# Kernel tuning notes

Hardware: AMD Instinct MI355X
Metric: run time of the kernel (lower is better)

The kernel has to match this reference:

```python
import jax, jax.numpy as jnp
import numpy as np

LN_EPS = 1e-5
B, T, H = 32, 1024, 1024


def _layer_norm(v, g, b):
    m = v.mean(-1, keepdims=True)
    var = ((v - m) ** 2).mean(-1, keepdims=True)
    return (v - m) / jnp.sqrt(var + LN_EPS) * g + b


def setup_inputs() -> dict:
    key = jax.random.key(0)
    ks = jax.random.split(key, 10)
    s_t = 1.0 / np.sqrt(T)
    s_h = 1.0 / np.sqrt(H)
    return {
        "x": jax.random.normal(ks[0], (B, T, H), jnp.float32),
        # temporal MLP (square T x T, triangular-masked), torch Linear layout [out, in]
        "tw1": jax.random.uniform(ks[1], (T, T), jnp.float32, -s_t, s_t),
        "tb1": jax.random.uniform(ks[2], (T,), jnp.float32, -s_t, s_t),
        "tw2": jax.random.uniform(ks[3], (T, T), jnp.float32, -s_t, s_t),
        "tb2": jax.random.uniform(ks[4], (T,), jnp.float32, -s_t, s_t),
        # channel MLP (square H x H)
        "cw1": jax.random.uniform(ks[5], (H, H), jnp.float32, -s_h, s_h),
        "cb1": jax.random.uniform(ks[6], (H,), jnp.float32, -s_h, s_h),
        "cw2": jax.random.uniform(ks[7], (H, H), jnp.float32, -s_h, s_h),
        "cb2": jax.random.uniform(ks[8], (H,), jnp.float32, -s_h, s_h),
        # LayerNorm affine params
        "ln1_g": jnp.ones((H,), jnp.float32),
        "ln1_b": jnp.zeros((H,), jnp.float32),
        "ln2_g": jnp.ones((H,), jnp.float32),
        "ln2_b": jnp.zeros((H,), jnp.float32),
    }


def reference(x, tw1, tb1, tw2, tb2, cw1, cb1, cw2, cb2, ln1_g, ln1_b, ln2_g, ln2_b):
    t = tw1.shape[0]
    mask = jnp.tril(jnp.ones((t, t), x.dtype))  # diagonal=0: include self
    # temporal mixing: LN -> swap -> masked Linear -> GELU -> masked Linear -> swap
    y = _layer_norm(x, ln1_g, ln1_b)
    y = jnp.swapaxes(y, 1, 2)  # [B, H, T]
    y = y @ (mask * tw1).T + tb1
    y = jax.nn.gelu(y, approximate=False)
    y = y @ (mask * tw2).T + tb2
    y = jnp.swapaxes(y, 1, 2)  # [B, T, H]
    x = x + y
    # channel mixing: LN -> Linear -> GELU -> Linear
    y2 = _layer_norm(x, ln2_g, ln2_b)
    y2 = jax.nn.gelu(y2 @ cw1.T + cb1, approximate=False) @ cw2.T + cb2
    return x + y2
```

## Files before the change

### kernel.cpp

```cpp
#include <hip/hip_runtime.h>
#include <hip/hip_bf16.h>

#define BDIM 32
#define TDIM 1024
#define HDIM 1024

typedef __attribute__((ext_vector_type(8))) short short8;
typedef __attribute__((ext_vector_type(8))) unsigned short ushort8;
typedef __attribute__((ext_vector_type(4))) unsigned short u16x4;
typedef __attribute__((ext_vector_type(4))) float f32x4;

__device__ __forceinline__ float b2f(unsigned short h){ return __uint_as_float(((unsigned)h)<<16); }
__device__ __forceinline__ unsigned short f2b(float f){
  unsigned u = __float_as_uint(f);
  u += 0x7fffu + ((u>>16)&1u);
  return (unsigned short)(u>>16);
}
__device__ __forceinline__ float gelu_f(float v){ return 0.5f*v*(1.0f+erff(v*0.70710678118f)); }
__device__ __forceinline__ void stv(float* p, float v){ *p = v; }
__device__ __forceinline__ void stv(unsigned short* p, float v){ *p = f2b(v); }

__global__ void prep_weights(const float* __restrict__ w1, const float* __restrict__ w2,
                             const float* __restrict__ c1, const float* __restrict__ c2,
                             unsigned short* __restrict__ w1m, unsigned short* __restrict__ w2m,
                             unsigned short* __restrict__ c1b, unsigned short* __restrict__ c2b){
  int idx = blockIdx.x*blockDim.x + threadIdx.x;
  int e = idx*4;
  int i = e >> 10, j0 = e & 1023;
  f32x4 a = *(const f32x4*)(w1+e);
  f32x4 b = *(const f32x4*)(w2+e);
  f32x4 c = *(const f32x4*)(c1+e);
  f32x4 d = *(const f32x4*)(c2+e);
  u16x4 av, bv, cv, dv;
  #pragma unroll
  for (int q=0;q<4;++q){
    float am = (j0+q <= i) ? a[q] : 0.f;
    float bm = (j0+q <= i) ? b[q] : 0.f;
    av[q]=f2b(am); bv[q]=f2b(bm); cv[q]=f2b(c[q]); dv[q]=f2b(d[q]);
  }
  *(u16x4*)(w1m+e)=av; *(u16x4*)(w2m+e)=bv; *(u16x4*)(c1b+e)=cv; *(u16x4*)(c2b+e)=dv;
}

__global__ __launch_bounds__(256) void ln1_stats_transpose(
    const float* __restrict__ x, const float* __restrict__ g, const float* __restrict__ bta,
    unsigned short* __restrict__ xnT){
  __shared__ float sm[64], sr[64];
  __shared__ float tile[64][65];
  const int t0 = blockIdx.x*64;
  const int b  = blockIdx.y;
  const int tid = threadIdx.x, wid = tid>>6, lane = tid&63;
  const size_t base = (size_t)b*TDIM*HDIM;
  for (int rr=0; rr<16; ++rr){
    int r = rr*4 + wid;
    const float* pr = x + base + (size_t)(t0+r)*HDIM;
    float s=0.f, s2=0.f;
    #pragma unroll
    for (int it=0; it<4; ++it){
      f32x4 v = *(const f32x4*)(pr + it*256 + lane*4);
      #pragma unroll
      for (int c=0;c<4;++c){ s += v[c]; s2 += v[c]*v[c]; }
    }
    #pragma unroll
    for (int off=32; off>0; off>>=1){ s += __shfl_xor(s,off,64); s2 += __shfl_xor(s2,off,64); }
    if (lane==0){
      float m = s * (1.0f/HDIM);
      sm[r] = m; sr[r] = rsqrtf(s2*(1.0f/HDIM) - m*m + 1e-5f);
    }
  }
  __syncthreads();
  const int rr = tid>>3, c8 = tid&7;
  for (int ht=0; ht<16; ++ht){
    int h0 = ht*64;
    #pragma unroll
    for (int p=0;p<2;++p){
      int r = rr + p*32;
      float m = sm[r], rs = sr[r];
      f32x4 v0 = *(const f32x4*)(x + base + (size_t)(t0+r)*HDIM + h0 + c8*8);
      f32x4 v1 = *(const f32x4*)(x + base + (size_t)(t0+r)*HDIM + h0 + c8*8 + 4);
      #pragma unroll
      for (int c=0;c<4;++c){
        int h = c8*8+c;
        tile[r][h]   = (v0[c]-m)*rs*g[h0+h]   + bta[h0+h];
        tile[r][h+4] = (v1[c]-m)*rs*g[h0+h+4] + bta[h0+h+4];
      }
    }
    __syncthreads();
    #pragma unroll
    for (int p=0;p<2;++p){
      int hr = rr + p*32;
      ushort8 ov;
      #pragma unroll
      for (int c=0;c<8;++c) ov[c] = f2b(tile[c8*8+c][hr]);
      *(ushort8*)(xnT + base + (size_t)(h0+hr)*TDIM + t0 + c8*8) = ov;
    }
    __syncthreads();
  }
}

__global__ void ln_fused(const unsigned short* __restrict__ p, const float* __restrict__ g,
                         const float* __restrict__ bta, unsigned short* __restrict__ o){
  int wid = threadIdx.x>>6, lane = threadIdx.x&63;
  size_t row = (size_t)blockIdx.x*4 + wid;
  const unsigned short* pr = p + row*HDIM + lane*16;
  ushort8 v0 = *(const ushort8*)(pr);
  ushort8 v1 = *(const ushort8*)(pr+8);
  float f[16];
  float s=0.f, s2=0.f;
  #pragma unroll
  for (int c=0;c<8;++c){ f[c]=b2f(v0[c]); f[c+8]=b2f(v1[c]); }
  #pragma unroll
  for (int c=0;c<16;++c){ s += f[c]; s2 += f[c]*f[c]; }
  #pragma unroll
  for (int off=32; off>0; off>>=1){ s += __shfl_xor(s,off,64); s2 += __shfl_xor(s2,off,64); }
  float m = s * (1.0f/HDIM);
  float rs = rsqrtf(s2*(1.0f/HDIM) - m*m + 1e-5f);
  int h0 = lane*16;
  ushort8 o0, o1;
  #pragma unroll
  for (int c=0;c<8;++c){
    o0[c] = f2b((f[c]-m)*rs*g[h0+c] + bta[h0+c]);
    o1[c] = f2b((f[c+8]-m)*rs*g[h0+c+8] + bta[h0+c+8]);
  }
  *(ushort8*)(o + row*HDIM + h0) = o0;
  *(ushort8*)(o + row*HDIM + h0 + 8) = o1;
}

template<int MODE, typename CT, typename RT>
__global__ __launch_bounds__(512,2)
void gemm256(const unsigned short* __restrict__ act, const unsigned short* __restrict__ wgt,
             CT* __restrict__ C, const float* __restrict__ bias, const RT* __restrict__ resid){
  extern __shared__ short S[];
  const int bid = blockIdx.x;
  const int tile = (bid & 7)*64 + (bid >> 3);
  const int panel = tile >> 2;
  const int inner = tile & 3;
  const unsigned short *pa, *pb;
  size_t cbase; int rg0, cg0, kend;
  if constexpr (MODE==1){
    int b = panel>>2, mt = panel&3;
    pa = act + (size_t)b*1048576 + (size_t)mt*262144;
    pb = wgt + (size_t)inner*262144;
    kend = (inner+1)*256;
    cbase = (size_t)b*1048576; rg0 = mt*256; cg0 = inner*256;
  } else if constexpr (MODE==2){
    int b = panel>>2, nt = panel&3;
    pa = wgt + (size_t)inner*262144;
    pb = act + (size_t)b*1048576 + (size_t)nt*262144;
    kend = (inner+1)*256;
    cbase = (size_t)b*1048576; rg0 = inner*256; cg0 = nt*256;
  } else {
    pa = act + (size_t)panel*262144;
    pb = wgt + (size_t)inner*262144;
    kend = 1024;
    cbase = 0; rg0 = panel*256; cg0 = inner*256;
  }
  const int tid = threadIdx.x;
  const int lane = tid & 63, wid = tid >> 6;
  const int wr = wid >> 2, wc = wid & 3;
  f32x4 acc[8][4];
  #pragma unroll
  for (int i=0;i<8;++i)
    #pragma unroll
    for (int j=0;j<4;++j) acc[i][j] = (f32x4)(0.f);

  const int NT = kend >> 6;
  const int Lb = tid*16;
  auto STAGE = [&](int buf, int k0){
    #pragma unroll
    for (int l=0;l<4;++l){
      int L = Lb + l*8192;
      int row = L >> 7;
      int ke  = (L & 127) >> 1;
      __builtin_amdgcn_global_load_lds(
        (const __attribute__((address_space(1))) void*)(pa + (size_t)row*1024 + k0 + ke),
        (__attribute__((address_space(3))) void*)((char*)S + buf*32768 + L), 16, 0, 0);
      __builtin_amdgcn_global_load_lds(
        (const __attribute__((address_space(1))) void*)(pb + (size_t)row*1024 + k0 + ke),
        (__attribute__((address_space(3))) void*)((char*)S + 65536 + buf*32768 + L), 16, 0, 0);
    }
  };

  const int arow = (wr*128 + (lane&15))*64 + (lane>>4)*8;
  const int brow = (wc*64  + (lane&15))*64 + (lane>>4)*8;

  STAGE(0, 0);
  __syncthreads();
  int cur = 0;
  for (int t=0; t<NT; ++t){
    if (t+1 < NT) STAGE(cur^1, (t+1)<<6);
    const short* Sa = S + cur*16384;
    const short* Sb = S + 32768 + cur*16384;
    #pragma unroll
    for (int s=0;s<2;++s){
      short8 af[8], bfv[4];
      #pragma unroll
      for (int i=0;i<8;++i) af[i] = *(const short8*)(Sa + arow + s*32 + i*1024);
      #pragma unroll
      for (int j=0;j<4;++j) bfv[j] = *(const short8*)(Sb + brow + s*32 + j*1024);
      #pragma unroll
      for (int i=0;i<8;++i)
        #pragma unroll
        for (int j=0;j<4;++j)
          acc[i][j] = __builtin_amdgcn_mfma_f32_16x16x32_bf16(af[i], bfv[j], acc[i][j], 0,0,0);
    }
    __syncthreads();
    cur ^= 1;
  }

  #pragma unroll
  for (int i=0;i<8;++i){
    int rbase = rg0 + wr*128 + i*16 + ((lane>>4)<<2);
    #pragma unroll
    for (int j=0;j<4;++j){
      int cg = cg0 + wc*64 + j*16 + (lane&15);
      float bn = (MODE!=2) ? bias[cg] : 0.f;
      #pragma unroll
      for (int r=0;r<4;++r){
        int rg = rbase + r;
        float v = acc[i][j][r];
        if (MODE==1 || MODE==3){ v += bn; v = gelu_f(v); }
        else if (MODE==2){ v += bias[rg]; v += resid[cbase + (size_t)rg*1024 + cg]; }
        else { v += bn; v += b2f(resid[cbase + (size_t)rg*1024 + cg]); }
        stv(&C[cbase + (size_t)rg*1024 + cg], v);
      }
    }
  }
}

extern "C" void kernel_launch(void* const* d_in, const int* in_sizes, int n_in,
                              void* d_out, int out_size, void* d_ws, size_t ws_size,
                              hipStream_t stream){
  const float* x    = (const float*)d_in[0];
  const float* tw1  = (const float*)d_in[1];
  const float* tb1  = (const float*)d_in[2];
  const float* tw2  = (const float*)d_in[3];
  const float* tb2  = (const float*)d_in[4];
  const float* cw1  = (const float*)d_in[5];
  const float* cb1  = (const float*)d_in[6];
  const float* cw2  = (const float*)d_in[7];
  const float* cb2  = (const float*)d_in[8];
  const float* g1   = (const float*)d_in[9];
  const float* bb1  = (const float*)d_in[10];
  const float* g2   = (const float*)d_in[11];
  const float* bb2  = (const float*)d_in[12];
  float* out = (float*)d_out;

  char* ws = (char*)d_ws;
  unsigned short* bufA = (unsigned short*)(ws);
  unsigned short* bufB = (unsigned short*)(ws + 67108864);
  unsigned short* xmid = (unsigned short*)(ws + 134217728);
  unsigned short* w1m  = (unsigned short*)(ws + 201326592);
  unsigned short* w2m  = (unsigned short*)(ws + 203423744);
  unsigned short* c1b  = (unsigned short*)(ws + 205520896);
  unsigned short* c2b  = (unsigned short*)(ws + 207618048);

  prep_weights<<<1024,256,0,stream>>>(tw1,tw2,cw1,cw2,w1m,w2m,c1b,c2b);
  ln1_stats_transpose<<<dim3(16,32),256,0,stream>>>(x, g1, bb1, bufA);
  gemm256<1,unsigned short,float><<<512,512,131072,stream>>>(bufA, w1m, bufB, tb1, (const float*)nullptr);
  gemm256<2,unsigned short,float><<<512,512,131072,stream>>>(bufB, w2m, xmid, tb2, x);
  ln_fused<<<8192,256,0,stream>>>(xmid, g2, bb2, bufA);
  gemm256<3,unsigned short,unsigned short><<<512,512,131072,stream>>>(bufA, c1b, bufB, cb1, (const unsigned short*)nullptr);
  gemm256<4,float,unsigned short><<<512,512,131072,stream>>>(bufB, c2b, out, cb2, xmid);
}
```

Before: 526.3 us.

## Restructure GEMM into quadrant-pipelined schedule with swizzled LDS and fine-grained waits

Replaces the double-buffered GEMM mainloop with a four-quadrant schedule. Each warp computes a 2x2 set of 64x32 sub-tiles, and global-to-LDS loads for the next stage are issued in quarter-tile chunks between MFMA groups, gated by explicit vmcnt waits and barriers. LDS rows are XOR-swizzled to avoid bank conflicts, and s_setprio raises priority around MFMA bursts. The aim is to overlap memory traffic with matrix math and cut LDS conflicts, at the cost of many more barriers per k-step and more fragile scheduling.

```diff
diff --git a/kernel.cpp b/kernel.cpp
--- a/kernel.cpp
+++ b/kernel.cpp
@@ -4,6 +4,8 @@
 #define BDIM 32
 #define TDIM 1024
 #define HDIM 1024
+#define AS1 __attribute__((address_space(1)))
+#define AS3 __attribute__((address_space(3)))
 
 typedef __attribute__((ext_vector_type(8))) short short8;
 typedef __attribute__((ext_vector_type(8))) unsigned short ushort8;
@@ -125,11 +127,16 @@
   *(ushort8*)(o + row*HDIM + h0 + 8) = o1;
 }
 
+#define GATE(N) do{ asm volatile("s_waitcnt vmcnt(" #N ")" ::: "memory"); \
+                    __builtin_amdgcn_sched_barrier(0); }while(0)
+#define BAR()   do{ __builtin_amdgcn_s_barrier(); \
+                    __builtin_amdgcn_sched_barrier(0); }while(0)
+
 template<int MODE, typename CT, typename RT>
 __global__ __launch_bounds__(512,2)
-void gemm256(const unsigned short* __restrict__ act, const unsigned short* __restrict__ wgt,
-             CT* __restrict__ C, const float* __restrict__ bias, const RT* __restrict__ resid){
-  extern __shared__ short S[];
+void gemmq(const unsigned short* __restrict__ act, const unsigned short* __restrict__ wgt,
+           CT* __restrict__ C, const float* __restrict__ bias, const RT* __restrict__ resid){
+  extern __shared__ char LDS[];
   const int bid = blockIdx.x;
   const int tile = (bid & 7)*64 + (bid >> 3);
   const int panel = tile >> 2;
@@ -154,70 +161,112 @@
     kend = 1024;
     cbase = 0; rg0 = panel*256; cg0 = inner*256;
   }
-  const int tid = threadIdx.x;
-  const int lane = tid & 63, wid = tid >> 6;
-  const int wr = wid >> 2, wc = wid & 3;
+  const int tid = threadIdx.x, lane = tid&63, wid = tid>>6;
+  const int wrow = (wid>>2)*64;
+  const int wcol = (wid&3)*32;
+  const int l15 = lane&15, l4b = (lane>>4)<<4;
   f32x4 acc[8][4];
   #pragma unroll
   for (int i=0;i<8;++i)
     #pragma unroll
     for (int j=0;j<4;++j) acc[i][j] = (f32x4)(0.f);
 
-  const int NT = kend >> 6;
-  const int Lb = tid*16;
-  auto STAGE = [&](int buf, int k0){
-    #pragma unroll
-    for (int l=0;l<4;++l){
-      int L = Lb + l*8192;
-      int row = L >> 7;
-      int ke  = (L & 127) >> 1;
+  const int NT = kend>>6;
+
+  auto STAGE = [&](int dt, int half, int st){
+    const unsigned short* src = (half<2) ? pa : pb;
+    const int rbase = (half&1)<<7;
+    char* dst = LDS + ((dt&1)<<16) + (half<<14);
+    const int k0 = st<<6;
+    #pragma unroll
+    for (int l=0;l<2;++l){
+      int W = tid*16 + (l<<13);
+      int r = W>>7;
+      int cs = (W&127) ^ ((r&7)<<4);
       __builtin_amdgcn_global_load_lds(
-        (const __attribute__((address_space(1))) void*)(pa + (size_t)row*1024 + k0 + ke),
-        (__attribute__((address_space(3))) void*)((char*)S + buf*32768 + L), 16, 0, 0);
-      __builtin_amdgcn_global_load_lds(
-        (const __attribute__((address_space(1))) void*)(pb + (size_t)row*1024 + k0 + ke),
-        (__attribute__((address_space(3))) void*)((char*)S + 65536 + buf*32768 + L), 16, 0, 0);
+        (const AS1 void*)(src + (size_t)(rbase+r)*1024 + k0 + (cs>>1)),
+        (AS3 void*)(dst + W), 16, 0, 0);
     }
   };
-
-  const int arow = (wr*128 + (lane&15))*64 + (lane>>4)*8;
-  const int brow = (wc*64  + (lane&15))*64 + (lane>>4)*8;
-
-  STAGE(0, 0);
-  __syncthreads();
-  int cur = 0;
+  auto STG = [&](int tt, int half, int t_now){ STAGE(tt, half, tt<NT ? tt : t_now); };
+
+  auto LDA = [&](int buf, int qa, int i, int s)->short8{
+    int ra = wrow + i*16 + l15;
+    int L = (ra<<7) + (((s<<6) + l4b) ^ ((ra&7)<<4));
+    return *(const short8*)(LDS + (buf<<16) + (qa<<14) + L);
+  };
+  auto LDB = [&](int buf, int qb, int j, int s)->short8{
+    int rb = wcol + j*16 + l15;
+    int L = (rb<<7) + (((s<<6) + l4b) ^ ((rb&7)<<4));
+    return *(const short8*)(LDS + (buf<<16) + ((2+qb)<<14) + L);
+  };
+
+  short8 aR[2][4], bR[2][2];
+
+#define MFMAQ(qa,qb)                                                         \
+  __builtin_amdgcn_s_setprio(1);                                             \
+  _Pragma("unroll") for (int s=0;s<2;++s)                                    \
+    _Pragma("unroll") for (int i=0;i<4;++i)                                  \
+      _Pragma("unroll") for (int j=0;j<2;++j)                                \
+        acc[(qa)*4+i][(qb)*2+j] = __builtin_amdgcn_mfma_f32_16x16x32_bf16(   \
+            aR[s][i], bR[s][j], acc[(qa)*4+i][(qb)*2+j], 0,0,0);             \
+  __builtin_amdgcn_s_setprio(0);
+
+  STAGE(0,0,0); STAGE(0,2,0); STAGE(0,1,0); STAGE(0,3,0);
+  STAGE(1,0, 1<NT ? 1 : 0);
+  GATE(6); BAR();
+
   for (int t=0; t<NT; ++t){
-    if (t+1 < NT) STAGE(cur^1, (t+1)<<6);
-    const short* Sa = S + cur*16384;
-    const short* Sb = S + 32768 + cur*16384;
+    const int buf = t&1;
     #pragma unroll
     for (int s=0;s<2;++s){
-      short8 af[8], bfv[4];
-      #pragma unroll
-      for (int i=0;i<8;++i) af[i] = *(const short8*)(Sa + arow + s*32 + i*1024);
-      #pragma unroll
-      for (int j=0;j<4;++j) bfv[j] = *(const short8*)(Sb + brow + s*32 + j*1024);
-      #pragma unroll
-      for (int i=0;i<8;++i)
-        #pragma unroll
-        for (int j=0;j<4;++j)
-          acc[i][j] = __builtin_amdgcn_mfma_f32_16x16x32_bf16(af[i], bfv[j], acc[i][j], 0,0,0);
-    }
-    __syncthreads();
-    cur ^= 1;
-  }
-
-  #pragma unroll
-  for (int i=0;i<8;++i){
-    int rbase = rg0 + wr*128 + i*16 + ((lane>>4)<<2);
-    #pragma unroll
-    for (int j=0;j<4;++j){
-      int cg = cg0 + wc*64 + j*16 + (lane&15);
+      #pragma unroll
+      for (int i=0;i<4;++i) aR[s][i] = LDA(buf,0,i,s);
+      #pragma unroll
+      for (int j=0;j<2;++j) bR[s][j] = LDB(buf,0,j,s);
+    }
+    STG(t+1, 2, t);
+    GATE(4); BAR();
+    MFMAQ(0,0)
+    BAR();
+    #pragma unroll
+    for (int s=0;s<2;++s)
+      #pragma unroll
+      for (int j=0;j<2;++j) bR[s][j] = LDB(buf,1,j,s);
+    STG(t+1, 1, t);
+    BAR();
+    MFMAQ(0,1)
+    BAR();
+    #pragma unroll
+    for (int s=0;s<2;++s)
+      #pragma unroll
+      for (int i=0;i<4;++i) aR[s][i] = LDA(buf,1,i,s);
+    STG(t+1, 3, t);
+    BAR();
+    MFMAQ(1,1)
+    BAR();
+    #pragma unroll
+    for (int s=0;s<2;++s)
+      #pragma unroll
+      for (int j=0;j<2;++j) bR[s][j] = LDB(buf,0,j,s);
+    STG(t+2, 0, t);
+    GATE(6); BAR();
+    MFMAQ(1,0)
+    BAR();
+  }
+#undef MFMAQ
+
+  #pragma unroll
+  for (int I=0;I<8;++I){
+    int rbase = rg0 + (I>>2)*128 + wrow + (I&3)*16 + ((lane>>4)<<2);
+    #pragma unroll
+    for (int J=0;J<4;++J){
+      int cg = cg0 + (J>>1)*128 + wcol + (J&1)*16 + l15;
       float bn = (MODE!=2) ? bias[cg] : 0.f;
       #pragma unroll
       for (int r=0;r<4;++r){
         int rg = rbase + r;
-        float v = acc[i][j][r];
+        float v = acc[I][J][r];
         if (MODE==1 || MODE==3){ v += bn; v = gelu_f(v); }
         else if (MODE==2){ v += bias[rg]; v += resid[cbase + (size_t)rg*1024 + cg]; }
         else { v += bn; v += b2f(resid[cbase + (size_t)rg*1024 + cg]); }
@@ -256,9 +305,9 @@
 
   prep_weights<<<1024,256,0,stream>>>(tw1,tw2,cw1,cw2,w1m,w2m,c1b,c2b);
   ln1_stats_transpose<<<dim3(16,32),256,0,stream>>>(x, g1, bb1, bufA);
-  gemm256<1,unsigned short,float><<<512,512,131072,stream>>>(bufA, w1m, bufB, tb1, (const float*)nullptr);
-  gemm256<2,unsigned short,float><<<512,512,131072,stream>>>(bufB, w2m, xmid, tb2, x);
+  gemmq<1,unsigned short,float><<<512,512,131072,stream>>>(bufA, w1m, bufB, tb1, (const float*)nullptr);
+  gemmq<2,unsigned short,float><<<512,512,131072,stream>>>(bufB, w2m, xmid, tb2, x);
   ln_fused<<<8192,256,0,stream>>>(xmid, g2, bb2, bufA);
-  gemm256<3,unsigned short,unsigned short><<<512,512,131072,stream>>>(bufA, c1b, bufB, cb1, (const unsigned short*)nullptr);
-  gemm256<4,float,unsigned short><<<512,512,131072,stream>>>(bufB, c2b, out, cb2, xmid);
-}
+  gemmq<3,unsigned short,unsigned short><<<512,512,131072,stream>>>(bufA, c1b, bufB, cb1, (const unsigned short*)nullptr);
+  gemmq<4,float,unsigned short><<<512,512,131072,stream>>>(bufB, c2b, out, cb2, xmid);
+}
```

Result: faster. 483.3 us (-8.2%).
